# Kernel tuning notes

Hardware: AMD Instinct MI355X
Metric: run time of the kernel (lower is better)

The kernel has to match this reference:

```python
import jax, jax.numpy as jnp
import numpy as np

N = 100_000
E = 1_600_000
IN_FT, HID, OUT = 512, 128, 64


def setup_inputs() -> dict:
    key = jax.random.key(0)
    ks = jax.random.split(key, 7)
    x = jax.random.normal(ks[0], (N, IN_FT), dtype=jnp.float32)
    edge_index = jax.random.randint(ks[1], (2, E), 0, N, dtype=jnp.int32)
    edge_weight = jax.random.uniform(ks[2], (E,), dtype=jnp.float32)
    W1 = jax.random.normal(ks[3], (IN_FT, HID), dtype=jnp.float32) * 0.05
    b1 = jnp.zeros((HID,), dtype=jnp.float32)
    W2 = jax.random.normal(ks[4], (HID, OUT), dtype=jnp.float32) * 0.05
    b2 = jnp.zeros((OUT,), dtype=jnp.float32)
    return {"x": x, "edge_index": edge_index, "edge_weight": edge_weight,
            "W1": W1, "b1": b1, "W2": W2, "b2": b2}


def reference(x, edge_index, edge_weight, W1, b1, W2, b2):
    n = x.shape[0]
    row, col = edge_index[0], edge_index[1]
    # PyG gcn_norm: add self-loops with weight 1, symmetric normalization
    loop = jnp.arange(n, dtype=row.dtype)
    r = jnp.concatenate([row, loop])
    c = jnp.concatenate([col, loop])
    w = jnp.concatenate([edge_weight, jnp.ones((n,), edge_weight.dtype)])
    deg = jax.ops.segment_sum(w, c, num_segments=n)
    dinv = jnp.where(deg > 0, jax.lax.rsqrt(deg), 0.0)
    norm = dinv[r] * w * dinv[c]  # [E + N]

    def conv(h, W, b):
        h = h @ W                                  # [N, F_out]
        msg = norm[:, None] * h[r]                 # gather source nodes
        return jax.ops.segment_sum(msg, c, num_segments=n) + b

    h = jax.nn.relu(conv(x, W1, b1))
    # dropout: inference mode (training=False) -> identity
    out = conv(h, W2, b2)
    return jax.nn.log_softmax(out, axis=1)
```

## Files before the change

kernel.cpp:

```cpp
#include <hip/hip_runtime.h>
#include <hip/hip_fp16.h>


constexpr int NN  = 100000;
constexpr int NE  = 1600000;
constexpr int FIN = 512;
constexpr int FH  = 128;
constexpr int FO  = 64;
constexpr int CAP = 64;

constexpr int NBLK1 = 512;
constexpr int EPB   = NE / NBLK1;
constexpr int NBKT  = 196;
constexpr int BCAP  = 9728;
constexpr int NWT   = FIN * FH + FH * FO;

constexpr float WSCALE  = 32767.0f;
constexpr float IWSCALE = 1.0f / 32767.0f;

typedef _Float16 f16x8 __attribute__((ext_vector_type(8)));
typedef float    f32x4 __attribute__((ext_vector_type(4)));

union F16Frag { short4 s[2]; f16x8 v; };


__global__ __launch_bounds__(256) void k_pass1(const int* __restrict__ rowi,
                                               const int* __restrict__ coli,
                                               const float* __restrict__ ew,
                                               const float* __restrict__ W1,
                                               const float* __restrict__ W2,
                                               _Float16* __restrict__ w1t,
                                               _Float16* __restrict__ w2t,
                                               int* __restrict__ bcur,
                                               unsigned long long* __restrict__ binned) {
    __shared__ unsigned long long buf[EPB];
    __shared__ int hist[NBKT];
    __shared__ int curs[NBKT];
    const int t = threadIdx.x;
    {
        int i = blockIdx.x * 256 + t;
        if (i < FIN * FH) {
            int k = i >> 7, c = i & 127;
            w1t[c * FIN + k] = (_Float16)W1[i];
        } else if (i < NWT) {
            int j = i - FIN * FH;
            int k = j >> 6, c = j & 63;
            w2t[c * FH + k] = (_Float16)W2[j];
        }
    }
    const int base = blockIdx.x * EPB;
    for (int i = t; i < NBKT; i += 256) hist[i] = 0;
    __syncthreads();
    for (int i = t; i < EPB; i += 256) {
        int e = base + i;
        int c = coli[e];
        unsigned wq = __float2uint_rn(ew[e] * WSCALE);
        buf[i] = ((unsigned long long)(unsigned)c << 32)
               | (unsigned long long)((wq << 17) | (unsigned)rowi[e]);
        atomicAdd(&hist[c >> 9], 1);
    }
    __syncthreads();
    if (t < NBKT) curs[t] = atomicAdd(&bcur[t], hist[t]);
    __syncthreads();
    for (int i = t; i < EPB; i += 256) {
        unsigned long long v = buf[i];
        int b = (int)(v >> 41);
        int pos = atomicAdd(&curs[b], 1);
        if ((unsigned)pos < BCAP) binned[(size_t)b * BCAP + pos] = v;
    }
}


__global__ __launch_bounds__(256) void k_pass2(const int* __restrict__ bcur,
                                               const unsigned long long* __restrict__ binned,
                                               unsigned* __restrict__ pay,
                                               int* __restrict__ cursor,
                                               float* __restrict__ dinv) {
    __shared__ int   cnt[512];
    __shared__ float wsum[512];
    const int t = threadIdx.x, b = blockIdx.x;
    for (int i = t; i < 512; i += 256) { cnt[i] = 0; wsum[i] = 0.f; }
    __syncthreads();
    const int total = min(bcur[b], BCAP);
    const int nbase = b * 512;
    for (int i = t; i < total; i += 256) {
        unsigned long long v = binned[(size_t)b * BCAP + i];
        int c9 = (int)((v >> 32) & 511);
        unsigned lo = (unsigned)v;
        int pos = atomicAdd(&cnt[c9], 1);
        atomicAdd(&wsum[c9], (float)(lo >> 17) * IWSCALE);
        if (pos < CAP) pay[(size_t)(nbase + c9) * CAP + pos] = lo;
    }
    __syncthreads();
    for (int i = t; i < 512; i += 256) {
        int node = nbase + i;
        if (node < NN) {
            cursor[node] = cnt[i];
            dinv[node]   = rsqrtf(1.0f + wsum[i]);
        }
    }
}


__global__ __launch_bounds__(256) void k_gemm1(const float* __restrict__ X,
                                               const _Float16* __restrict__ w1t,
                                               _Float16* __restrict__ H1) {
    __shared__ __align__(16) _Float16 As[64 * 64];
    __shared__ __align__(16) _Float16 Bs[128 * 64];
    const int tid  = threadIdx.x;
    const int nwg = gridDim.x;
    const int q = nwg >> 3, r = nwg & 7;
    const int xcd = blockIdx.x & 7, idx = blockIdx.x >> 3;
    const int wg = (xcd < r ? xcd * (q + 1) : r * (q + 1) + (xcd - r) * q) + idx;
    const int brow = wg * 64;
    const int wid = tid >> 6, l = tid & 63;
    const int wr = wid >> 1, wc = wid & 1;
    const int l15 = l & 15, lg = l >> 4;

    f32x4 acc[2][4];
#pragma unroll
    for (int m = 0; m < 2; ++m)
#pragma unroll
        for (int n = 0; n < 4; ++n) acc[m][n] = (f32x4){0.f, 0.f, 0.f, 0.f};

    const int ar    = tid >> 2;
    const int apart = tid & 3;
    const int grow  = brow + ar;
    const int br    = tid >> 1;
    const int bhalf = tid & 1;

    for (int k0 = 0; k0 < FIN; k0 += 64) {
#pragma unroll
        for (int h = 0; h < 2; ++h) {
            int slot = apart * 2 + h;
            float4 lo = make_float4(0.f, 0.f, 0.f, 0.f), hi = lo;
            if (grow < NN) {
                lo = *(const float4*)&X[(size_t)grow * FIN + k0 + slot * 8];
                hi = *(const float4*)&X[(size_t)grow * FIN + k0 + slot * 8 + 4];
            }
            union { _Float16 f[8]; int4 v; } pk;
            pk.f[0] = (_Float16)lo.x; pk.f[1] = (_Float16)lo.y;
            pk.f[2] = (_Float16)lo.z; pk.f[3] = (_Float16)lo.w;
            pk.f[4] = (_Float16)hi.x; pk.f[5] = (_Float16)hi.y;
            pk.f[6] = (_Float16)hi.z; pk.f[7] = (_Float16)hi.w;
            *(int4*)&As[ar * 64 + ((slot ^ (ar & 7)) * 8)] = pk.v;
        }
#pragma unroll
        for (int j = 0; j < 4; ++j) {
            int slot = bhalf * 4 + j;
            *(int4*)&Bs[br * 64 + ((slot ^ (br & 7)) * 8)] =
                *(const int4*)&w1t[br * FIN + k0 + slot * 8];
        }
        __syncthreads();
#pragma unroll
        for (int ks = 0; ks < 2; ++ks) {
            F16Frag au[2], bu[4];
            int klo = ks * 32 + 4 * lg;
            int khi = klo + 16;
#pragma unroll
            for (int m = 0; m < 2; ++m) {
                int row = wr * 32 + m * 16 + l15;
                int sw  = row & 7;
                au[m].s[0] = *(const short4*)&As[row * 64 + (((klo >> 3) ^ sw) * 8) + (klo & 7)];
                au[m].s[1] = *(const short4*)&As[row * 64 + (((khi >> 3) ^ sw) * 8) + (khi & 7)];
            }
#pragma unroll
            for (int n = 0; n < 4; ++n) {
                int row = wc * 64 + n * 16 + l15;
                int sw  = row & 7;
                bu[n].s[0] = *(const short4*)&Bs[row * 64 + (((klo >> 3) ^ sw) * 8) + (klo & 7)];
                bu[n].s[1] = *(const short4*)&Bs[row * 64 + (((khi >> 3) ^ sw) * 8) + (khi & 7)];
            }
#pragma unroll
            for (int m = 0; m < 2; ++m)
#pragma unroll
                for (int n = 0; n < 4; ++n)
                    acc[m][n] = __builtin_amdgcn_mfma_f32_16x16x32_f16(
                        au[m].v, bu[n].v, acc[m][n], 0, 0, 0);
        }
        __syncthreads();
    }
#pragma unroll
    for (int m = 0; m < 2; ++m)
#pragma unroll
        for (int n = 0; n < 4; ++n) {
            int gcol = wc * 64 + n * 16 + l15;
#pragma unroll
            for (int r4 = 0; r4 < 4; ++r4) {
                int gr = brow + wr * 32 + m * 16 + lg * 4 + r4;
                if (gr < NN) H1[(size_t)gr * FH + gcol] = (_Float16)acc[m][n][r4];
            }
        }
}


__global__ __launch_bounds__(256) void k_gemm2(const _Float16* __restrict__ H2,
                                               const _Float16* __restrict__ w2t,
                                               _Float16* __restrict__ H3) {
    __shared__ __align__(16) _Float16 As[64 * 128];
    __shared__ __align__(16) _Float16 Bs[64 * 128];
    const int tid  = threadIdx.x;
    const int brow = blockIdx.x * 64;
    const int wid = tid >> 6, l = tid & 63;
    const int wr = wid >> 1, wc = wid & 1;
    const int l15 = l & 15, lg = l >> 4;

    f32x4 acc[2][2];
#pragma unroll
    for (int m = 0; m < 2; ++m)
#pragma unroll
        for (int n = 0; n < 2; ++n) acc[m][n] = (f32x4){0.f, 0.f, 0.f, 0.f};

    {
        int ar = tid >> 2, part = tid & 3, grow = brow + ar;
#pragma unroll
        for (int j = 0; j < 4; ++j) {
            int slot = part * 4 + j;
            int4 v = make_int4(0, 0, 0, 0);
            if (grow < NN) v = *(const int4*)&H2[(size_t)grow * FH + slot * 8];
            *(int4*)&As[ar * 128 + ((slot ^ (ar & 15)) * 8)] = v;
            *(int4*)&Bs[ar * 128 + ((slot ^ (ar & 15)) * 8)] =
                *(const int4*)&w2t[ar * FH + slot * 8];
        }
    }
    __syncthreads();
#pragma unroll
    for (int ks = 0; ks < 4; ++ks) {
        F16Frag au[2], bu[2];
        int klo = ks * 32 + 4 * lg;
        int khi = klo + 16;
#pragma unroll
        for (int m = 0; m < 2; ++m) {
            int row = wr * 32 + m * 16 + l15;
            int sw  = row & 15;
            au[m].s[0] = *(const short4*)&As[row * 128 + (((klo >> 3) ^ sw) * 8) + (klo & 7)];
            au[m].s[1] = *(const short4*)&As[row * 128 + (((khi >> 3) ^ sw) * 8) + (khi & 7)];
        }
#pragma unroll
        for (int n = 0; n < 2; ++n) {
            int row = wc * 32 + n * 16 + l15;
            int sw  = row & 15;
            bu[n].s[0] = *(const short4*)&Bs[row * 128 + (((klo >> 3) ^ sw) * 8) + (klo & 7)];
            bu[n].s[1] = *(const short4*)&Bs[row * 128 + (((khi >> 3) ^ sw) * 8) + (khi & 7)];
        }
#pragma unroll
        for (int m = 0; m < 2; ++m)
#pragma unroll
            for (int n = 0; n < 2; ++n)
                acc[m][n] = __builtin_amdgcn_mfma_f32_16x16x32_f16(
                    au[m].v, bu[n].v, acc[m][n], 0, 0, 0);
    }
#pragma unroll
    for (int m = 0; m < 2; ++m)
#pragma unroll
        for (int n = 0; n < 2; ++n) {
            int gcol = wc * 32 + n * 16 + l15;
#pragma unroll
            for (int r4 = 0; r4 < 4; ++r4) {
                int gr = brow + wr * 32 + m * 16 + lg * 4 + r4;
                if (gr < NN) H3[(size_t)gr * FO + gcol] = (_Float16)acc[m][n][r4];
            }
        }
}


__global__ __launch_bounds__(256) void k_agg1(const int* __restrict__ cursor,
                                              const unsigned* __restrict__ pay,
                                              const float* __restrict__ dinv,
                                              const __half* __restrict__ H1,
                                              const float* __restrict__ b1,
                                              __half* __restrict__ H2) {
    int node = (blockIdx.x * 256 + threadIdx.x) >> 6;
    int lane = threadIdx.x & 63;
    if (node >= NN) return;
    const int f = lane * 2;
    float dc  = dinv[node];
    float dcs = dc * IWSCALE;
    float2 hc = __half22float2(*(const __half2*)&H1[(size_t)node * FH + f]);
    float a0x = dc * dc * hc.x, a0y = dc * dc * hc.y;
    float a1x = 0, a1y = 0, a2x = 0, a2y = 0, a3x = 0, a3y = 0;
    int cnt = min(max(cursor[node], 0), CAP);
    const unsigned* p = &pay[(size_t)node * CAP];
    int e = 0;
    for (; e + 8 <= cnt; e += 8) {
        uint4 pa = *(const uint4*)&p[e];
        uint4 pb = *(const uint4*)&p[e + 4];
        int s0 = pa.x & 0x1FFFF, s1 = pa.y & 0x1FFFF, s2 = pa.z & 0x1FFFF, s3 = pa.w & 0x1FFFF;
        int s4 = pb.x & 0x1FFFF, s5 = pb.y & 0x1FFFF, s6 = pb.z & 0x1FFFF, s7 = pb.w & 0x1FFFF;
        float w0 = (float)(pa.x >> 17) * dcs * dinv[s0];
        float w1 = (float)(pa.y >> 17) * dcs * dinv[s1];
        float w2 = (float)(pa.z >> 17) * dcs * dinv[s2];
        float w3 = (float)(pa.w >> 17) * dcs * dinv[s3];
        float w4 = (float)(pb.x >> 17) * dcs * dinv[s4];
        float w5 = (float)(pb.y >> 17) * dcs * dinv[s5];
        float w6 = (float)(pb.z >> 17) * dcs * dinv[s6];
        float w7 = (float)(pb.w >> 17) * dcs * dinv[s7];
        float2 g0 = __half22float2(*(const __half2*)&H1[(size_t)s0 * FH + f]);
        float2 g1 = __half22float2(*(const __half2*)&H1[(size_t)s1 * FH + f]);
        float2 g2 = __half22float2(*(const __half2*)&H1[(size_t)s2 * FH + f]);
        float2 g3 = __half22float2(*(const __half2*)&H1[(size_t)s3 * FH + f]);
        float2 g4 = __half22float2(*(const __half2*)&H1[(size_t)s4 * FH + f]);
        float2 g5 = __half22float2(*(const __half2*)&H1[(size_t)s5 * FH + f]);
        float2 g6 = __half22float2(*(const __half2*)&H1[(size_t)s6 * FH + f]);
        float2 g7 = __half22float2(*(const __half2*)&H1[(size_t)s7 * FH + f]);
        a0x += w0 * g0.x; a0y += w0 * g0.y;  a1x += w1 * g1.x; a1y += w1 * g1.y;
        a2x += w2 * g2.x; a2y += w2 * g2.y;  a3x += w3 * g3.x; a3y += w3 * g3.y;
        a0x += w4 * g4.x; a0y += w4 * g4.y;  a1x += w5 * g5.x; a1y += w5 * g5.y;
        a2x += w6 * g6.x; a2y += w6 * g6.y;  a3x += w7 * g7.x; a3y += w7 * g7.y;
    }
    for (; e < cnt; ++e) {
        unsigned v = p[e];
        int s = v & 0x1FFFF;
        float w = (float)(v >> 17) * dcs * dinv[s];
        float2 g = __half22float2(*(const __half2*)&H1[(size_t)s * FH + f]);
        a0x += w * g.x; a0y += w * g.y;
    }
    float vx = a0x + a1x + a2x + a3x + b1[f];
    float vy = a0y + a1y + a2y + a3y + b1[f + 1];
    vx = vx > 0.f ? vx : 0.f;
    vy = vy > 0.f ? vy : 0.f;
    *(__half2*)&H2[(size_t)node * FH + f] = __floats2half2_rn(vx, vy);
}


__global__ __launch_bounds__(256) void k_agg2(const int* __restrict__ cursor,
                                              const unsigned* __restrict__ pay,
                                              const float* __restrict__ dinv,
                                              const __half* __restrict__ H3,
                                              const float* __restrict__ b2,
                                              float* __restrict__ out) {
    int node = (blockIdx.x * 256 + threadIdx.x) >> 6;
    int lane = threadIdx.x & 63;
    if (node >= NN) return;
    float dc  = dinv[node];
    float dcs = dc * IWSCALE;
    float a0 = dc * dc * __half2float(H3[(size_t)node * FO + lane]);
    float a1 = 0, a2 = 0, a3 = 0;
    int cnt = min(max(cursor[node], 0), CAP);
    const unsigned* p = &pay[(size_t)node * CAP];
    int e = 0;
    for (; e + 8 <= cnt; e += 8) {
        uint4 pa = *(const uint4*)&p[e];
        uint4 pb = *(const uint4*)&p[e + 4];
        int s0 = pa.x & 0x1FFFF, s1 = pa.y & 0x1FFFF, s2 = pa.z & 0x1FFFF, s3 = pa.w & 0x1FFFF;
        int s4 = pb.x & 0x1FFFF, s5 = pb.y & 0x1FFFF, s6 = pb.z & 0x1FFFF, s7 = pb.w & 0x1FFFF;
        float w0 = (float)(pa.x >> 17) * dcs * dinv[s0];
        float w1 = (float)(pa.y >> 17) * dcs * dinv[s1];
        float w2 = (float)(pa.z >> 17) * dcs * dinv[s2];
        float w3 = (float)(pa.w >> 17) * dcs * dinv[s3];
        float w4 = (float)(pb.x >> 17) * dcs * dinv[s4];
        float w5 = (float)(pb.y >> 17) * dcs * dinv[s5];
        float w6 = (float)(pb.z >> 17) * dcs * dinv[s6];
        float w7 = (float)(pb.w >> 17) * dcs * dinv[s7];
        a0 += w0 * __half2float(H3[(size_t)s0 * FO + lane]);
        a1 += w1 * __half2float(H3[(size_t)s1 * FO + lane]);
        a2 += w2 * __half2float(H3[(size_t)s2 * FO + lane]);
        a3 += w3 * __half2float(H3[(size_t)s3 * FO + lane]);
        a0 += w4 * __half2float(H3[(size_t)s4 * FO + lane]);
        a1 += w5 * __half2float(H3[(size_t)s5 * FO + lane]);
        a2 += w6 * __half2float(H3[(size_t)s6 * FO + lane]);
        a3 += w7 * __half2float(H3[(size_t)s7 * FO + lane]);
    }
    for (; e < cnt; ++e) {
        unsigned v = p[e];
        int s = v & 0x1FFFF;
        float w = (float)(v >> 17) * dcs * dinv[s];
        a0 += w * __half2float(H3[(size_t)s * FO + lane]);
    }
    float v = a0 + a1 + a2 + a3 + b2[lane];
    float m = v;
#pragma unroll
    for (int s = 32; s; s >>= 1) m = fmaxf(m, __shfl_xor(m, s));
    float ex = expf(v - m);
    float sum = ex;
#pragma unroll
    for (int s = 32; s; s >>= 1) sum += __shfl_xor(sum, s);
    out[(size_t)node * FO + lane] = v - m - logf(sum);
}


extern "C" void kernel_launch(void* const* d_in, const int* in_sizes, int n_in,
                              void* d_out, int out_size, void* d_ws, size_t ws_size,
                              hipStream_t stream) {
    const float* x   = (const float*)d_in[0];
    const int*   ei  = (const int*)d_in[1];
    const int*   row = ei;
    const int*   col = ei + NE;
    const float* ew  = (const float*)d_in[2];
    const float* W1  = (const float*)d_in[3];
    const float* b1  = (const float*)d_in[4];
    const float* W2  = (const float*)d_in[5];
    const float* b2  = (const float*)d_in[6];
    float* out = (float*)d_out;

    int*       bcur   = (int*)d_ws;
    int*       cursor = bcur + 256;
    float*     dinv   = (float*)(cursor + 102400);
    _Float16*  w1t    = (_Float16*)(dinv + 102400);
    _Float16*  w2t    = w1t + FIN * FH;
    unsigned long long* binned = (unsigned long long*)(w2t + FH * FO);
    unsigned*  pay    = (unsigned*)(binned + (size_t)NBKT * BCAP);
    _Float16*  H1     = (_Float16*)(pay + (size_t)NN * CAP);
    _Float16*  H2     = H1 + (size_t)NN * FH;
    _Float16*  H3     = H2 + (size_t)NN * FH;

    hipMemsetAsync(bcur, 0, NBKT * sizeof(int), stream);
    k_pass1<<<NBLK1, 256, 0, stream>>>(row, col, ew, W1, W2, w1t, w2t, bcur, binned);
    k_pass2<<<NBKT, 256, 0, stream>>>(bcur, binned, pay, cursor, dinv);

    k_gemm1<<<(NN + 63) / 64, 256, 0, stream>>>(x, w1t, H1);
    k_agg1 <<<(NN * 64 + 255) / 256, 256, 0, stream>>>(cursor, pay, dinv,
                                                       (const __half*)H1, b1, (__half*)H2);
    k_gemm2<<<(NN + 63) / 64, 256, 0, stream>>>(H2, w2t, H3);
    k_agg2 <<<(NN * 64 + 255) / 256, 256, 0, stream>>>(cursor, pay, dinv,
                                                       (const __half*)H3, b2, out);
}
```

Baseline: 282.4 us.

## Double-buffer GEMM1 LDS tiles and prefetch next K tile into registers

The first-layer GEMM now uses two LDS buffers and issues the global loads for the next K tile into registers before running the MFMA work on the current tile. This hides global load latency behind compute and drops one barrier per iteration. Out-of-range rows are clamped to the last valid row rather than zero-filled; those rows are never stored. It costs double the LDS (48KB per block), which may lower occupancy, plus extra registers for the prefetched data.

```diff
diff --git a/kernel.cpp b/kernel.cpp
--- a/kernel.cpp
+++ b/kernel.cpp
@@ -105,8 +105,8 @@
 __global__ __launch_bounds__(256) void k_gemm1(const float* __restrict__ X,
                                                const _Float16* __restrict__ w1t,
                                                _Float16* __restrict__ H1) {
-    __shared__ __align__(16) _Float16 As[64 * 64];
-    __shared__ __align__(16) _Float16 Bs[128 * 64];
+    __shared__ __align__(16) _Float16 As[2][64 * 64];
+    __shared__ __align__(16) _Float16 Bs[2][128 * 64];
     const int tid  = threadIdx.x;
     const int nwg = gridDim.x;
     const int q = nwg >> 3, r = nwg & 7;
@@ -125,33 +125,51 @@
 
     const int ar    = tid >> 2;
     const int apart = tid & 3;
-    const int grow  = brow + ar;
+    const int grow  = min(brow + ar, NN - 1);
     const int br    = tid >> 1;
     const int bhalf = tid & 1;
 
-    for (int k0 = 0; k0 < FIN; k0 += 64) {
+    float4 xa[4];
+    int4   wb[4];
+
+    auto load_tile = [&](int k0) {
 #pragma unroll
         for (int h = 0; h < 2; ++h) {
             int slot = apart * 2 + h;
-            float4 lo = make_float4(0.f, 0.f, 0.f, 0.f), hi = lo;
-            if (grow < NN) {
-                lo = *(const float4*)&X[(size_t)grow * FIN + k0 + slot * 8];
-                hi = *(const float4*)&X[(size_t)grow * FIN + k0 + slot * 8 + 4];
-            }
-            union { _Float16 f[8]; int4 v; } pk;
-            pk.f[0] = (_Float16)lo.x; pk.f[1] = (_Float16)lo.y;
-            pk.f[2] = (_Float16)lo.z; pk.f[3] = (_Float16)lo.w;
-            pk.f[4] = (_Float16)hi.x; pk.f[5] = (_Float16)hi.y;
-            pk.f[6] = (_Float16)hi.z; pk.f[7] = (_Float16)hi.w;
-            *(int4*)&As[ar * 64 + ((slot ^ (ar & 7)) * 8)] = pk.v;
+            xa[h * 2]     = *(const float4*)&X[(size_t)grow * FIN + k0 + slot * 8];
+            xa[h * 2 + 1] = *(const float4*)&X[(size_t)grow * FIN + k0 + slot * 8 + 4];
         }
 #pragma unroll
         for (int j = 0; j < 4; ++j) {
             int slot = bhalf * 4 + j;
-            *(int4*)&Bs[br * 64 + ((slot ^ (br & 7)) * 8)] =
-                *(const int4*)&w1t[br * FIN + k0 + slot * 8];
-        }
+            wb[j] = *(const int4*)&w1t[br * FIN + k0 + slot * 8];
+        }
+    };
+    auto write_tile = [&](int buf) {
+#pragma unroll
+        for (int h = 0; h < 2; ++h) {
+            int slot = apart * 2 + h;
+            union { _Float16 f[8]; int4 v; } pk;
+            float4 a = xa[h * 2], b = xa[h * 2 + 1];
+            pk.f[0] = (_Float16)a.x; pk.f[1] = (_Float16)a.y;
+            pk.f[2] = (_Float16)a.z; pk.f[3] = (_Float16)a.w;
+            pk.f[4] = (_Float16)b.x; pk.f[5] = (_Float16)b.y;
+            pk.f[6] = (_Float16)b.z; pk.f[7] = (_Float16)b.w;
+            *(int4*)&As[buf][ar * 64 + ((slot ^ (ar & 7)) * 8)] = pk.v;
+        }
+#pragma unroll
+        for (int j = 0; j < 4; ++j) {
+            int slot = bhalf * 4 + j;
+            *(int4*)&Bs[buf][br * 64 + ((slot ^ (br & 7)) * 8)] = wb[j];
+        }
+    };
+
+    load_tile(0);
+    for (int t = 0; t < 8; ++t) {
+        const int buf = t & 1;
+        write_tile(buf);
         __syncthreads();
+        if (t < 7) load_tile((t + 1) * 64);
 #pragma unroll
         for (int ks = 0; ks < 2; ++ks) {
             F16Frag au[2], bu[4];
@@ -161,15 +179,15 @@
             for (int m = 0; m < 2; ++m) {
                 int row = wr * 32 + m * 16 + l15;
                 int sw  = row & 7;
-                au[m].s[0] = *(const short4*)&As[row * 64 + (((klo >> 3) ^ sw) * 8) + (klo & 7)];
-                au[m].s[1] = *(const short4*)&As[row * 64 + (((khi >> 3) ^ sw) * 8) + (khi & 7)];
+                au[m].s[0] = *(const short4*)&As[buf][row * 64 + (((klo >> 3) ^ sw) * 8) + (klo & 7)];
+                au[m].s[1] = *(const short4*)&As[buf][row * 64 + (((khi >> 3) ^ sw) * 8) + (khi & 7)];
             }
 #pragma unroll
             for (int n = 0; n < 4; ++n) {
                 int row = wc * 64 + n * 16 + l15;
                 int sw  = row & 7;
-                bu[n].s[0] = *(const short4*)&Bs[row * 64 + (((klo >> 3) ^ sw) * 8) + (klo & 7)];
-                bu[n].s[1] = *(const short4*)&Bs[row * 64 + (((khi >> 3) ^ sw) * 8) + (khi & 7)];
+                bu[n].s[0] = *(const short4*)&Bs[buf][row * 64 + (((klo >> 3) ^ sw) * 8) + (klo & 7)];
+                bu[n].s[1] = *(const short4*)&Bs[buf][row * 64 + (((khi >> 3) ^ sw) * 8) + (khi & 7)];
             }
 #pragma unroll
             for (int m = 0; m < 2; ++m)
@@ -178,7 +196,6 @@
                     acc[m][n] = __builtin_amdgcn_mfma_f32_16x16x32_f16(
                         au[m].v, bu[n].v, acc[m][n], 0, 0, 0);
         }
-        __syncthreads();
     }
 #pragma unroll
     for (int m = 0; m < 2; ++m)
```

Result: slower. 316.6 us (+12.1%).

## Load GEMM MFMA fragments directly from global memory, dropping LDS staging

Applied to the files above, without the earlier changes.

Both dense GEMM kernels stop staging A and B tiles through shared memory and instead have each lane load its MFMA fragment straight from global memory (with fp32→fp16 conversion in registers for X). This removes the LDS writes, reads and barriers. gemm2 also gives each wave a full 32x64 output tile with 128 rows per block. The risk is that the per-lane loads are strided and narrow (16–32 bytes per row), so sectors may be underused and B rows are reloaded by every wave. The XCD-aware block remapping in gemm1 is also dropped.

```diff
diff --git a/kernel.cpp b/kernel.cpp
--- a/kernel.cpp
+++ b/kernel.cpp
@@ -21,7 +21,7 @@
 typedef _Float16 f16x8 __attribute__((ext_vector_type(8)));
 typedef float    f32x4 __attribute__((ext_vector_type(4)));
 
-union F16Frag { short4 s[2]; f16x8 v; };
+union F16Frag { _Float16 f[8]; short4 s[2]; f16x8 v; };
 
 
 __global__ __launch_bounds__(256) void k_pass1(const int* __restrict__ rowi,
@@ -105,17 +105,11 @@
 __global__ __launch_bounds__(256) void k_gemm1(const float* __restrict__ X,
                                                const _Float16* __restrict__ w1t,
                                                _Float16* __restrict__ H1) {
-    __shared__ __align__(16) _Float16 As[64 * 64];
-    __shared__ __align__(16) _Float16 Bs[128 * 64];
-    const int tid  = threadIdx.x;
-    const int nwg = gridDim.x;
-    const int q = nwg >> 3, r = nwg & 7;
-    const int xcd = blockIdx.x & 7, idx = blockIdx.x >> 3;
-    const int wg = (xcd < r ? xcd * (q + 1) : r * (q + 1) + (xcd - r) * q) + idx;
-    const int brow = wg * 64;
+    const int tid = threadIdx.x;
     const int wid = tid >> 6, l = tid & 63;
     const int wr = wid >> 1, wc = wid & 1;
     const int l15 = l & 15, lg = l >> 4;
+    const int brow = blockIdx.x * 64;
 
     f32x4 acc[2][4];
 #pragma unroll
@@ -123,62 +117,39 @@
 #pragma unroll
         for (int n = 0; n < 4; ++n) acc[m][n] = (f32x4){0.f, 0.f, 0.f, 0.f};
 
-    const int ar    = tid >> 2;
-    const int apart = tid & 3;
-    const int grow  = brow + ar;
-    const int br    = tid >> 1;
-    const int bhalf = tid & 1;
-
-    for (int k0 = 0; k0 < FIN; k0 += 64) {
-#pragma unroll
-        for (int h = 0; h < 2; ++h) {
-            int slot = apart * 2 + h;
-            float4 lo = make_float4(0.f, 0.f, 0.f, 0.f), hi = lo;
-            if (grow < NN) {
-                lo = *(const float4*)&X[(size_t)grow * FIN + k0 + slot * 8];
-                hi = *(const float4*)&X[(size_t)grow * FIN + k0 + slot * 8 + 4];
-            }
-            union { _Float16 f[8]; int4 v; } pk;
-            pk.f[0] = (_Float16)lo.x; pk.f[1] = (_Float16)lo.y;
-            pk.f[2] = (_Float16)lo.z; pk.f[3] = (_Float16)lo.w;
-            pk.f[4] = (_Float16)hi.x; pk.f[5] = (_Float16)hi.y;
-            pk.f[6] = (_Float16)hi.z; pk.f[7] = (_Float16)hi.w;
-            *(int4*)&As[ar * 64 + ((slot ^ (ar & 7)) * 8)] = pk.v;
-        }
-#pragma unroll
-        for (int j = 0; j < 4; ++j) {
-            int slot = bhalf * 4 + j;
-            *(int4*)&Bs[br * 64 + ((slot ^ (br & 7)) * 8)] =
-                *(const int4*)&w1t[br * FIN + k0 + slot * 8];
-        }
-        __syncthreads();
-#pragma unroll
-        for (int ks = 0; ks < 2; ++ks) {
-            F16Frag au[2], bu[4];
-            int klo = ks * 32 + 4 * lg;
-            int khi = klo + 16;
-#pragma unroll
-            for (int m = 0; m < 2; ++m) {
-                int row = wr * 32 + m * 16 + l15;
-                int sw  = row & 7;
-                au[m].s[0] = *(const short4*)&As[row * 64 + (((klo >> 3) ^ sw) * 8) + (klo & 7)];
-                au[m].s[1] = *(const short4*)&As[row * 64 + (((khi >> 3) ^ sw) * 8) + (khi & 7)];
-            }
-#pragma unroll
-            for (int n = 0; n < 4; ++n) {
-                int row = wc * 64 + n * 16 + l15;
-                int sw  = row & 7;
-                bu[n].s[0] = *(const short4*)&Bs[row * 64 + (((klo >> 3) ^ sw) * 8) + (klo & 7)];
-                bu[n].s[1] = *(const short4*)&Bs[row * 64 + (((khi >> 3) ^ sw) * 8) + (khi & 7)];
-            }
-#pragma unroll
-            for (int m = 0; m < 2; ++m)
-#pragma unroll
-                for (int n = 0; n < 4; ++n)
-                    acc[m][n] = __builtin_amdgcn_mfma_f32_16x16x32_f16(
-                        au[m].v, bu[n].v, acc[m][n], 0, 0, 0);
-        }
-        __syncthreads();
+    const float* pa[2];
+#pragma unroll
+    for (int m = 0; m < 2; ++m)
+        pa[m] = &X[(size_t)min(brow + wr * 32 + m * 16 + l15, NN - 1) * FIN];
+    const _Float16* pb[4];
+#pragma unroll
+    for (int n = 0; n < 4; ++n)
+        pb[n] = &w1t[(size_t)(wc * 64 + n * 16 + l15) * FIN];
+
+    for (int ks = 0; ks < 16; ++ks) {
+        const int klo = ks * 32 + 4 * lg;
+        const int khi = klo + 16;
+        F16Frag au[2], bu[4];
+#pragma unroll
+        for (int m = 0; m < 2; ++m) {
+            float4 lo = *(const float4*)&pa[m][klo];
+            float4 hi = *(const float4*)&pa[m][khi];
+            au[m].f[0] = (_Float16)lo.x; au[m].f[1] = (_Float16)lo.y;
+            au[m].f[2] = (_Float16)lo.z; au[m].f[3] = (_Float16)lo.w;
+            au[m].f[4] = (_Float16)hi.x; au[m].f[5] = (_Float16)hi.y;
+            au[m].f[6] = (_Float16)hi.z; au[m].f[7] = (_Float16)hi.w;
+        }
+#pragma unroll
+        for (int n = 0; n < 4; ++n) {
+            bu[n].s[0] = *(const short4*)&pb[n][klo];
+            bu[n].s[1] = *(const short4*)&pb[n][khi];
+        }
+#pragma unroll
+        for (int m = 0; m < 2; ++m)
+#pragma unroll
+            for (int n = 0; n < 4; ++n)
+                acc[m][n] = __builtin_amdgcn_mfma_f32_16x16x32_f16(
+                    au[m].v, bu[n].v, acc[m][n], 0, 0, 0);
     }
 #pragma unroll
     for (int m = 0; m < 2; ++m)
@@ -197,67 +168,55 @@
 __global__ __launch_bounds__(256) void k_gemm2(const _Float16* __restrict__ H2,
                                                const _Float16* __restrict__ w2t,
                                                _Float16* __restrict__ H3) {
-    __shared__ __align__(16) _Float16 As[64 * 128];
-    __shared__ __align__(16) _Float16 Bs[64 * 128];
-    const int tid  = threadIdx.x;
-    const int brow = blockIdx.x * 64;
+    const int tid = threadIdx.x;
     const int wid = tid >> 6, l = tid & 63;
-    const int wr = wid >> 1, wc = wid & 1;
     const int l15 = l & 15, lg = l >> 4;
-
-    f32x4 acc[2][2];
-#pragma unroll
-    for (int m = 0; m < 2; ++m)
-#pragma unroll
-        for (int n = 0; n < 2; ++n) acc[m][n] = (f32x4){0.f, 0.f, 0.f, 0.f};
-
-    {
-        int ar = tid >> 2, part = tid & 3, grow = brow + ar;
-#pragma unroll
-        for (int j = 0; j < 4; ++j) {
-            int slot = part * 4 + j;
-            int4 v = make_int4(0, 0, 0, 0);
-            if (grow < NN) v = *(const int4*)&H2[(size_t)grow * FH + slot * 8];
-            *(int4*)&As[ar * 128 + ((slot ^ (ar & 15)) * 8)] = v;
-            *(int4*)&Bs[ar * 128 + ((slot ^ (ar & 15)) * 8)] =
-                *(const int4*)&w2t[ar * FH + slot * 8];
-        }
-    }
-    __syncthreads();
-#pragma unroll
+    const int wrow = blockIdx.x * 128 + wid * 32;
+
+    f32x4 acc[2][4];
+#pragma unroll
+    for (int m = 0; m < 2; ++m)
+#pragma unroll
+        for (int n = 0; n < 4; ++n) acc[m][n] = (f32x4){0.f, 0.f, 0.f, 0.f};
+
+    const _Float16* pa[2];
+#pragma unroll
+    for (int m = 0; m < 2; ++m)
+        pa[m] = &H2[(size_t)min(wrow + m * 16 + l15, NN - 1) * FH];
+    const _Float16* pb[4];
+#pragma unroll
+    for (int n = 0; n < 4; ++n)
+        pb[n] = &w2t[(size_t)(n * 16 + l15) * FH];
+
     for (int ks = 0; ks < 4; ++ks) {
-        F16Frag au[2], bu[2];
-        int klo = ks * 32 + 4 * lg;
-        int khi = klo + 16;
+        const int klo = ks * 32 + 4 * lg;
+        const int khi = klo + 16;
+        F16Frag au[2], bu[4];
 #pragma unroll
         for (int m = 0; m < 2; ++m) {
-            int row = wr * 32 + m * 16 + l15;
-            int sw  = row & 15;
-            au[m].s[0] = *(const short4*)&As[row * 128 + (((klo >> 3) ^ sw) * 8) + (klo & 7)];
-            au[m].s[1] = *(const short4*)&As[row * 128 + (((khi >> 3) ^ sw) * 8) + (khi & 7)];
-        }
-#pragma unroll
-        for (int n = 0; n < 2; ++n) {
-            int row = wc * 32 + n * 16 + l15;
-            int sw  = row & 15;
-            bu[n].s[0] = *(const short4*)&Bs[row * 128 + (((klo >> 3) ^ sw) * 8) + (klo & 7)];
-            bu[n].s[1] = *(const short4*)&Bs[row * 128 + (((khi >> 3) ^ sw) * 8) + (khi & 7)];
+            au[m].s[0] = *(const short4*)&pa[m][klo];
+            au[m].s[1] = *(const short4*)&pa[m][khi];
+        }
+#pragma unroll
+        for (int n = 0; n < 4; ++n) {
+            bu[n].s[0] = *(const short4*)&pb[n][klo];
+            bu[n].s[1] = *(const short4*)&pb[n][khi];
         }
 #pragma unroll
         for (int m = 0; m < 2; ++m)
 #pragma unroll
-            for (int n = 0; n < 2; ++n)
+            for (int n = 0; n < 4; ++n)
                 acc[m][n] = __builtin_amdgcn_mfma_f32_16x16x32_f16(
                     au[m].v, bu[n].v, acc[m][n], 0, 0, 0);
     }
 #pragma unroll
     for (int m = 0; m < 2; ++m)
 #pragma unroll
-        for (int n = 0; n < 2; ++n) {
-            int gcol = wc * 32 + n * 16 + l15;
+        for (int n = 0; n < 4; ++n) {
+            int gcol = n * 16 + l15;
 #pragma unroll
             for (int r4 = 0; r4 < 4; ++r4) {
-                int gr = brow + wr * 32 + m * 16 + lg * 4 + r4;
+                int gr = wrow + m * 16 + lg * 4 + r4;
                 if (gr < NN) H3[(size_t)gr * FO + gcol] = (_Float16)acc[m][n][r4];
             }
         }
@@ -411,7 +370,7 @@
     k_gemm1<<<(NN + 63) / 64, 256, 0, stream>>>(x, w1t, H1);
     k_agg1 <<<(NN * 64 + 255) / 256, 256, 0, stream>>>(cursor, pay, dinv,
                                                        (const __half*)H1, b1, (__half*)H2);
-    k_gemm2<<<(NN + 63) / 64, 256, 0, stream>>>(H2, w2t, H3);
+    k_gemm2<<<(NN + 127) / 128, 256, 0, stream>>>(H2, w2t, H3);
     k_agg2 <<<(NN * 64 + 255) / 256, 256, 0, stream>>>(cursor, pay, dinv,
                                                        (const __half*)H3, b2, out);
 }
```

After: 384.6 us. 36.2% more time.

## Load GEMM1 tiles directly into LDS via global_load_lds, convert fp32 at fragment read

Applied to the files above, without the earlier changes.

The first GEMM now streams X tiles as fp32 and W1 tiles straight from global memory into shared memory with direct global-to-LDS loads. This bypasses the register round trip, and the fp16 conversion moves to the fragment read. The XCD-aware block remapping is dropped and out-of-range rows are clamped rather than zero-filled. The cost is double the LDS footprint for the A tile and repeated conversion work in the inner loop.

```diff
diff --git a/kernel.cpp b/kernel.cpp
--- a/kernel.cpp
+++ b/kernel.cpp
@@ -21,7 +21,14 @@
 typedef _Float16 f16x8 __attribute__((ext_vector_type(8)));
 typedef float    f32x4 __attribute__((ext_vector_type(4)));
 
-union F16Frag { short4 s[2]; f16x8 v; };
+union F16Frag { _Float16 f[8]; short4 s[2]; f16x8 v; };
+
+__device__ __forceinline__ void gload16(const void* g, void* l) {
+    __builtin_amdgcn_global_load_lds(
+        (const __attribute__((address_space(1))) void*)g,
+        (__attribute__((address_space(3))) void*)l,
+        16, 0, 0);
+}
 
 
 __global__ __launch_bounds__(256) void k_pass1(const int* __restrict__ rowi,
@@ -105,17 +112,13 @@
 __global__ __launch_bounds__(256) void k_gemm1(const float* __restrict__ X,
                                                const _Float16* __restrict__ w1t,
                                                _Float16* __restrict__ H1) {
-    __shared__ __align__(16) _Float16 As[64 * 64];
+    __shared__ __align__(16) float    Asf[64 * 64];
     __shared__ __align__(16) _Float16 Bs[128 * 64];
-    const int tid  = threadIdx.x;
-    const int nwg = gridDim.x;
-    const int q = nwg >> 3, r = nwg & 7;
-    const int xcd = blockIdx.x & 7, idx = blockIdx.x >> 3;
-    const int wg = (xcd < r ? xcd * (q + 1) : r * (q + 1) + (xcd - r) * q) + idx;
-    const int brow = wg * 64;
+    const int tid = threadIdx.x;
     const int wid = tid >> 6, l = tid & 63;
     const int wr = wid >> 1, wc = wid & 1;
     const int l15 = l & 15, lg = l >> 4;
+    const int brow = blockIdx.x * 64;
 
     f32x4 acc[2][4];
 #pragma unroll
@@ -123,53 +126,48 @@
 #pragma unroll
         for (int n = 0; n < 4; ++n) acc[m][n] = (f32x4){0.f, 0.f, 0.f, 0.f};
 
-    const int ar    = tid >> 2;
-    const int apart = tid & 3;
-    const int grow  = brow + ar;
-    const int br    = tid >> 1;
-    const int bhalf = tid & 1;
+    const int rA = wid * 16 + (l >> 4);
+    const int sA = l & 15;
+    const int rB = wid * 32 + (l >> 3);
+    const int sB = l & 7;
 
     for (int k0 = 0; k0 < FIN; k0 += 64) {
 #pragma unroll
-        for (int h = 0; h < 2; ++h) {
-            int slot = apart * 2 + h;
-            float4 lo = make_float4(0.f, 0.f, 0.f, 0.f), hi = lo;
-            if (grow < NN) {
-                lo = *(const float4*)&X[(size_t)grow * FIN + k0 + slot * 8];
-                hi = *(const float4*)&X[(size_t)grow * FIN + k0 + slot * 8 + 4];
-            }
-            union { _Float16 f[8]; int4 v; } pk;
-            pk.f[0] = (_Float16)lo.x; pk.f[1] = (_Float16)lo.y;
-            pk.f[2] = (_Float16)lo.z; pk.f[3] = (_Float16)lo.w;
-            pk.f[4] = (_Float16)hi.x; pk.f[5] = (_Float16)hi.y;
-            pk.f[6] = (_Float16)hi.z; pk.f[7] = (_Float16)hi.w;
-            *(int4*)&As[ar * 64 + ((slot ^ (ar & 7)) * 8)] = pk.v;
-        }
-#pragma unroll
         for (int j = 0; j < 4; ++j) {
-            int slot = bhalf * 4 + j;
-            *(int4*)&Bs[br * 64 + ((slot ^ (br & 7)) * 8)] =
-                *(const int4*)&w1t[br * FIN + k0 + slot * 8];
+            int r  = rA + j * 4;
+            int sg = sA ^ (r & 15);
+            gload16(&X[(size_t)min(brow + r, NN - 1) * FIN + k0 + sg * 4],
+                    &Asf[wid * 1024 + j * 256]);
+        }
+#pragma unroll
+        for (int j = 0; j < 4; ++j) {
+            int r  = rB + j * 8;
+            int sg = sB ^ (r & 7);
+            gload16(&w1t[(size_t)r * FIN + k0 + sg * 8],
+                    &Bs[wid * 2048 + j * 512]);
         }
         __syncthreads();
 #pragma unroll
         for (int ks = 0; ks < 2; ++ks) {
             F16Frag au[2], bu[4];
-            int klo = ks * 32 + 4 * lg;
-            int khi = klo + 16;
 #pragma unroll
             for (int m = 0; m < 2; ++m) {
                 int row = wr * 32 + m * 16 + l15;
-                int sw  = row & 7;
-                au[m].s[0] = *(const short4*)&As[row * 64 + (((klo >> 3) ^ sw) * 8) + (klo & 7)];
-                au[m].s[1] = *(const short4*)&As[row * 64 + (((khi >> 3) ^ sw) * 8) + (khi & 7)];
+                int slo = ks * 8 + lg;
+                float4 lo = *(const float4*)&Asf[row * 64 + ((slo       ^ (row & 15)) * 4)];
+                float4 hi = *(const float4*)&Asf[row * 64 + (((slo + 4) ^ (row & 15)) * 4)];
+                au[m].f[0] = (_Float16)lo.x; au[m].f[1] = (_Float16)lo.y;
+                au[m].f[2] = (_Float16)lo.z; au[m].f[3] = (_Float16)lo.w;
+                au[m].f[4] = (_Float16)hi.x; au[m].f[5] = (_Float16)hi.y;
+                au[m].f[6] = (_Float16)hi.z; au[m].f[7] = (_Float16)hi.w;
             }
 #pragma unroll
             for (int n = 0; n < 4; ++n) {
                 int row = wc * 64 + n * 16 + l15;
-                int sw  = row & 7;
-                bu[n].s[0] = *(const short4*)&Bs[row * 64 + (((klo >> 3) ^ sw) * 8) + (klo & 7)];
-                bu[n].s[1] = *(const short4*)&Bs[row * 64 + (((khi >> 3) ^ sw) * 8) + (khi & 7)];
+                int sb  = ks * 4 + (lg >> 1);
+                int wi  = (lg & 1) * 4;
+                bu[n].s[0] = *(const short4*)&Bs[row * 64 + ((sb       ^ (row & 7)) * 8) + wi];
+                bu[n].s[1] = *(const short4*)&Bs[row * 64 + (((sb + 2) ^ (row & 7)) * 8) + wi];
             }
 #pragma unroll
             for (int m = 0; m < 2; ++m)
```

Result: faster. 261.6 us (-7.4%).
